# Optimization experiments

Measured on AMD Instinct MI355X. Metric: run time of the kernel, lower is better.

Reference implementation:

```python
import jax, jax.numpy as jnp
import numpy as np

NUM_LAYERS = 2

def setup_inputs() -> dict:
    key = jax.random.key(0)
    ks = jax.random.split(key, 10)
    N, E, V, D, G = 50000, 800000, 100000, 128, 64
    node_ids = jax.random.randint(ks[0], (N,), 0, V)
    edge_index = jax.random.randint(ks[1], (2, E), 0, N)
    batch = jnp.sort(jax.random.randint(ks[2], (N,), 0, G))
    embed = jax.random.normal(ks[3], (V, D), dtype=jnp.float32)
    conv_w = jax.random.normal(ks[4], (NUM_LAYERS, D, D), dtype=jnp.float32) * (1.0 / np.sqrt(D))
    w_ih = jax.random.normal(ks[5], (3 * D, D), dtype=jnp.float32) * (1.0 / np.sqrt(D))
    w_hh = jax.random.normal(ks[6], (3 * D, D), dtype=jnp.float32) * (1.0 / np.sqrt(D))
    b_ih = jax.random.normal(ks[7], (3 * D,), dtype=jnp.float32) * 0.01
    b_hh = jax.random.normal(ks[8], (3 * D,), dtype=jnp.float32) * 0.01
    return {"node_ids": node_ids, "edge_index": edge_index, "batch": batch,
            "num_graphs": 64, "embed": embed, "conv_w": conv_w,
            "w_ih": w_ih, "w_hh": w_hh, "b_ih": b_ih, "b_hh": b_hh}


def _gru_cell(x, h, w_ih, w_hh, b_ih, b_hh):
    # torch.nn.GRUCell math; gate order r, z, n
    gi = x @ w_ih.T + b_ih
    gh = h @ w_hh.T + b_hh
    i_r, i_z, i_n = jnp.split(gi, 3, axis=-1)
    h_r, h_z, h_n = jnp.split(gh, 3, axis=-1)
    r = jax.nn.sigmoid(i_r + h_r)
    z = jax.nn.sigmoid(i_z + h_z)
    n = jnp.tanh(i_n + r * h_n)
    return (1.0 - z) * n + z * h


def reference(node_ids, edge_index, batch, num_graphs, embed, conv_w, w_ih, w_hh, b_ih, b_hh):
    N = node_ids.shape[0]
    src, dst = edge_index[0], edge_index[1]
    h = embed[node_ids]  # [N, D]
    for i in range(NUM_LAYERS):
        m = h @ conv_w[i]                                   # [N, D]
        agg = jax.ops.segment_sum(m[src], dst, num_segments=N)  # scatter-add messages
        h = _gru_cell(agg, h, w_ih, w_hh, b_ih, b_hh)
    # global mean pool per graph
    sums = jax.ops.segment_sum(h, batch, num_segments=num_graphs)       # [G, D]
    counts = jax.ops.segment_sum(jnp.ones((N,), h.dtype), batch, num_segments=num_graphs)
    return sums / jnp.maximum(counts, 1.0)[:, None]
```

## Files before the change

### kernel.cpp

```cpp
#include <hip/hip_runtime.h>
#include <hip/hip_bf16.h>


#define DTHREADS 256
#define BSHIFT 7
#define BNODES 128
#define BCAP 4096

typedef __attribute__((ext_vector_type(8))) short bf16x8;
typedef __attribute__((ext_vector_type(4))) float f32x4;

__device__ __forceinline__ float sigf(float x) { return 1.0f / (1.0f + __expf(-x)); }
__device__ __forceinline__ float tanhfast(float x) { return 1.0f - 2.0f / (1.0f + __expf(2.0f * x)); }

__device__ __forceinline__ unsigned short f2bf_rne(float x) {
  unsigned int u = __float_as_uint(x);
  u += 0x7fff + ((u >> 16) & 1);
  return (unsigned short)(u >> 16);
}
__device__ __forceinline__ float bf2f(unsigned int lo16) {
  return __uint_as_float(lo16 << 16);
}

__global__ __launch_bounds__(DTHREADS) void gather_kernel(
    const float* __restrict__ embed, const int* __restrict__ node_ids,
    unsigned short* __restrict__ hb, int N) {
  int idx = blockIdx.x * DTHREADS + threadIdx.x;
  if (idx >= N * 32) return;
  int n = idx >> 5;
  int c = (idx & 31) * 4;
  int v = node_ids[n];
  float4 val = *(const float4*)&embed[(size_t)v * 128 + c];
  unsigned short b[4] = {f2bf_rne(val.x), f2bf_rne(val.y), f2bf_rne(val.z), f2bf_rne(val.w)};
  *(ushort4*)&hb[(size_t)n * 128 + c] = *(ushort4*)b;
}

__global__ __launch_bounds__(DTHREADS) void pack_all_kernel(
    const float* __restrict__ w_hh, const float* __restrict__ conv_w,
    const float* __restrict__ w_ih, unsigned short* __restrict__ wpk_hh,
    unsigned short* __restrict__ wpk_wc, int nl,
    int* __restrict__ cur, int NB, float* __restrict__ outsum, int osz) {
  int id = blockIdx.x * DTHREADS + threadIdx.x;
  if (id < NB) cur[id] = 0;
  if (id < osz) outsum[id] = 0.f;
  int seg = id / (384 * 128);
  if (seg > nl) return;
  int r = id - seg * (384 * 128);
  int f = r >> 3, i = r & 7;
  int l = f & 63;
  int s = (f >> 6) & 3;
  int t = (f >> 8) & 3;
  int jb = f >> 10;
  int j = jb * 64 + t * 16 + (l & 15);
  int k = s * 32 + (l >> 4) * 8 + i;
  float val;
  unsigned short* dst;
  if (seg == 0) {
    val = w_hh[j * 128 + k];
    dst = wpk_hh;
  } else {
    const float* conv = conv_w + (size_t)(seg - 1) * 128 * 128;
    float acc = 0.f;
    for (int d = 0; d < 128; d += 4) {
      float4 cv = *(const float4*)&conv[k * 128 + d];
      float4 wv = *(const float4*)&w_ih[j * 128 + d];
      acc += cv.x * wv.x + cv.y * wv.y + cv.z * wv.z + cv.w * wv.w;
    }
    val = acc;
    dst = wpk_wc + (size_t)(seg - 1) * 384 * 128;
  }
  dst[(size_t)f * 8 + i] = f2bf_rne(val);
}

__global__ __launch_bounds__(DTHREADS) void bucket_scatter_kernel(
    const int* __restrict__ src, const int* __restrict__ dst,
    int* __restrict__ cur, unsigned int* __restrict__ ebuf, int E, int NB) {
  __shared__ int lc[512];
  __shared__ int lbs[512];
  int tid = threadIdx.x;
  for (int i = tid; i < NB; i += DTHREADS) lc[i] = 0;
  __syncthreads();
  int base = blockIdx.x * 4096;
  int rank[16];
  #pragma unroll
  for (int q = 0; q < 16; ++q) {
    int e = base + q * 256 + tid;
    if (e < E) rank[q] = atomicAdd(&lc[dst[e] >> BSHIFT], 1);
  }
  __syncthreads();
  for (int i = tid; i < NB; i += DTHREADS) {
    int c = lc[i];
    lbs[i] = c ? atomicAdd(&cur[i], c) : 0;
  }
  __syncthreads();
  #pragma unroll
  for (int q = 0; q < 16; ++q) {
    int e = base + q * 256 + tid;
    if (e < E) {
      int d = dst[e];
      int b = d >> BSHIFT;
      int slot = lbs[b] + rank[q];
      if (slot < BCAP)
        ebuf[(size_t)b * BCAP + slot] =
            (unsigned int)src[e] | ((unsigned int)(d & (BNODES - 1)) << 17);
    }
  }
}

__global__ __launch_bounds__(DTHREADS) void bucket_sort_kernel(
    const unsigned int* __restrict__ ebuf, const int* __restrict__ cur,
    int* __restrict__ row_start, int* __restrict__ row_end,
    int* __restrict__ csr_src, int N) {
  __shared__ int cnt[BNODES];
  __shared__ int sc[BNODES];
  const int tid = threadIdx.x;
  const int b = blockIdx.x;
  const int count = min(cur[b], BCAP);
  const unsigned int* eb = ebuf + (size_t)b * BCAP;
  int* cs = csr_src + (size_t)b * BCAP;
  if (tid < BNODES) cnt[tid] = 0;
  __syncthreads();
  for (int i = tid; i < count; i += DTHREADS)
    atomicAdd(&cnt[eb[i] >> 17], 1);
  __syncthreads();
  if (tid < BNODES) sc[tid] = cnt[tid];
  __syncthreads();
  #pragma unroll
  for (int off = 1; off < BNODES; off <<= 1) {
    int t = 0;
    if (tid < BNODES && tid >= off) t = sc[tid - off];
    __syncthreads();
    if (tid < BNODES) sc[tid] += t;
    __syncthreads();
  }
  if (tid < BNODES) {
    int excl = sc[tid] - cnt[tid];
    int n = b * BNODES + tid;
    if (n < N) {
      row_start[n] = b * BCAP + excl;
      row_end[n] = b * BCAP + sc[tid];
    }
    cnt[tid] = excl;
  }
  __syncthreads();
  for (int i = tid; i < count; i += DTHREADS) {
    unsigned int pk = eb[i];
    int slot = atomicAdd(&cnt[pk >> 17], 1);
    cs[slot] = (int)(pk & 0x1FFFFu);
  }
}

__global__ __launch_bounds__(DTHREADS) void aggregate_kernel(
    const unsigned short* __restrict__ hb, const int* __restrict__ row_start,
    const int* __restrict__ row_end, const int* __restrict__ csr_src,
    unsigned short* __restrict__ agg, int N) {
  int node = (blockIdx.x * DTHREADS + threadIdx.x) >> 4;
  if (node >= N) return;
  int c = threadIdx.x & 15;
  int s = row_start[node], e = row_end[node];
  float acc[8] = {0.f, 0.f, 0.f, 0.f, 0.f, 0.f, 0.f, 0.f};
  for (int i = s; i < e; i += 16) {
    int idx[16];
    #pragma unroll
    for (int q = 0; q < 16; ++q) {
      int ii = i + q;
      idx[q] = csr_src[ii < e ? ii : s];
    }
    uint4 d[16];
    #pragma unroll
    for (int q = 0; q < 16; ++q)
      d[q] = *(const uint4*)&hb[(size_t)idx[q] * 128 + c * 8];
    #pragma unroll
    for (int q = 0; q < 16; ++q) {
      if (i + q < e) {
        const unsigned int* dp = (const unsigned int*)&d[q];
        #pragma unroll
        for (int u = 0; u < 4; ++u) {
          acc[2 * u]     += bf2f(dp[u] & 0xffffu);
          acc[2 * u + 1] += bf2f(dp[u] >> 16);
        }
      }
    }
  }
  unsigned int o[4];
  #pragma unroll
  for (int q = 0; q < 4; ++q)
    o[q] = (unsigned int)f2bf_rne(acc[2 * q]) | ((unsigned int)f2bf_rne(acc[2 * q + 1]) << 16);
  *(uint4*)&agg[(size_t)node * 128 + c * 8] = *(uint4*)o;
}

__global__ __launch_bounds__(512, 2) void fused_gru_kernel(
    const unsigned short* __restrict__ aggb, const unsigned short* __restrict__ wpk_wc,
    const unsigned short* __restrict__ wpk_hh, const float* __restrict__ b_ih,
    const float* __restrict__ b_hh, unsigned short* __restrict__ hb,
    int N, int nchunks) {
  __shared__ __align__(16) unsigned short Ag[32 * 128];
  __shared__ __align__(16) unsigned short Hs[32 * 128];
  const int tid = threadIdx.x;
  const int wv = tid >> 6, lane = tid & 63;
  const int lm = lane & 15, quad = lane >> 4;

  bf16x8 BI[3][4], BH[3][4];
  #pragma unroll
  for (int g = 0; g < 3; ++g) {
    int jb = g * 2 + (wv >> 2);
    int t = wv & 3;
    #pragma unroll
    for (int s = 0; s < 4; ++s) {
      size_t f = ((size_t)(jb * 4 + t) * 4 + s) * 64 + lane;
      BI[g][s] = *(const bf16x8*)&wpk_wc[f * 8];
      BH[g][s] = *(const bf16x8*)&wpk_hh[f * 8];
    }
  }

  const int jc = wv * 16 + lm;
  const float bir = b_ih[jc], biz = b_ih[128 + jc], bin_ = b_ih[256 + jc];
  const float bhr = b_hh[jc], bhz = b_hh[128 + jc], bhn = b_hh[256 + jc];
  const int c0 = jc >> 3, ej = jc & 7;

  const int srow = tid >> 4, scol = tid & 15;
  const int sdc = (scol ^ (srow & 15)) * 8;

  int ci = blockIdx.x;
  uint4 va = make_uint4(0, 0, 0, 0), vh = make_uint4(0, 0, 0, 0);
  if (ci < nchunks) {
    int n = ci * 32 + srow;
    if (n < N) {
      va = *(const uint4*)&aggb[(size_t)n * 128 + scol * 8];
      vh = *(const uint4*)&hb[(size_t)n * 128 + scol * 8];
    }
  }

  for (; ci < nchunks; ci += gridDim.x) {
    *(uint4*)&Ag[srow * 128 + sdc] = va;
    *(uint4*)&Hs[srow * 128 + sdc] = vh;
    __syncthreads();

    int cn = ci + gridDim.x;
    va = make_uint4(0, 0, 0, 0); vh = make_uint4(0, 0, 0, 0);
    if (cn < nchunks) {
      int n = cn * 32 + srow;
      if (n < N) {
        va = *(const uint4*)&aggb[(size_t)n * 128 + scol * 8];
        vh = *(const uint4*)&hb[(size_t)n * 128 + scol * 8];
      }
    }

    f32x4 accI[2][3], accH[2][3];
    #pragma unroll
    for (int mi = 0; mi < 2; ++mi)
      #pragma unroll
      for (int g = 0; g < 3; ++g) {
        accI[mi][g] = (f32x4){0.f, 0.f, 0.f, 0.f};
        accH[mi][g] = (f32x4){0.f, 0.f, 0.f, 0.f};
      }

    #pragma unroll
    for (int s = 0; s < 4; ++s) {
      bf16x8 afA[2], afH[2];
      #pragma unroll
      for (int mi = 0; mi < 2; ++mi) {
        int m = mi * 16 + lm;
        int chunk = (s * 4 + quad) ^ (m & 15);
        afA[mi] = *(const bf16x8*)&Ag[m * 128 + chunk * 8];
        afH[mi] = *(const bf16x8*)&Hs[m * 128 + chunk * 8];
      }
      #pragma unroll
      for (int g = 0; g < 3; ++g)
        #pragma unroll
        for (int mi = 0; mi < 2; ++mi) {
          accI[mi][g] = __builtin_amdgcn_mfma_f32_16x16x32_bf16(afA[mi], BI[g][s], accI[mi][g], 0, 0, 0);
          accH[mi][g] = __builtin_amdgcn_mfma_f32_16x16x32_bf16(afH[mi], BH[g][s], accH[mi][g], 0, 0, 0);
        }
    }

    const int n0 = ci * 32;
    #pragma unroll
    for (int mi = 0; mi < 2; ++mi) {
      #pragma unroll
      for (int r = 0; r < 4; ++r) {
        int row = mi * 16 + quad * 4 + r;
        int n = n0 + row;
        if (n >= N) continue;
        float ir = accI[mi][0][r] + bir;
        float iz = accI[mi][1][r] + biz;
        float in_ = accI[mi][2][r] + bin_;
        float hr = accH[mi][0][r] + bhr;
        float hz = accH[mi][1][r] + bhz;
        float hn = accH[mi][2][r] + bhn;
        float rr = sigf(ir + hr);
        float zz = sigf(iz + hz);
        float nn = tanhfast(in_ + rr * hn);
        float hold = bf2f((unsigned int)Hs[row * 128 + ((c0 ^ (row & 15)) * 8) + ej]);
        hb[(size_t)n * 128 + jc] = f2bf_rne((1.f - zz) * nn + zz * hold);
      }
    }
    __syncthreads();
  }
}

__global__ __launch_bounds__(DTHREADS) void pool1_kernel(
    const unsigned short* __restrict__ hb, const int* __restrict__ batch,
    float* __restrict__ outsum, int N) {
  int b = blockIdx.x;
  int c = threadIdx.x & 127;
  int half = threadIdx.x >> 7;
  int nbeg = b * 64;
  int nend = min(nbeg + 64, N);
  float acc = 0.f;
  int cur = -1;
  for (int n = nbeg + half; n < nend; n += 2) {
    int g = batch[n];
    if (g != cur) {
      if (cur >= 0) atomicAdd(&outsum[(size_t)cur * 128 + c], acc);
      acc = 0.f;
      cur = g;
    }
    acc += bf2f((unsigned int)hb[(size_t)n * 128 + c]);
  }
  if (cur >= 0) atomicAdd(&outsum[(size_t)cur * 128 + c], acc);
}

__device__ __forceinline__ int lbound(const int* a, int n, int key) {
  int lo = 0, hi = n;
  while (lo < hi) {
    int mid = (lo + hi) >> 1;
    if (a[mid] < key) lo = mid + 1; else hi = mid;
  }
  return lo;
}

__global__ __launch_bounds__(128) void pool2_kernel(
    const float* __restrict__ outsum, const int* __restrict__ batch,
    float* __restrict__ out, int N) {
  int g = blockIdx.x;
  int c = threadIdx.x;
  int lo = lbound(batch, N, g);
  int hi = lbound(batch, N, g + 1);
  out[(size_t)g * 128 + c] = outsum[(size_t)g * 128 + c] / (float)max(hi - lo, 1);
}

extern "C" void kernel_launch(void* const* d_in, const int* in_sizes, int n_in,
                              void* d_out, int out_size, void* d_ws, size_t ws_size,
                              hipStream_t stream) {
  const int* node_ids = (const int*)d_in[0];
  const int* edge_index = (const int*)d_in[1];
  const int* batch = (const int*)d_in[2];
  const float* embed = (const float*)d_in[4];
  const float* conv_w = (const float*)d_in[5];
  const float* w_ih = (const float*)d_in[6];
  const float* w_hh = (const float*)d_in[7];
  const float* b_ih = (const float*)d_in[8];
  const float* b_hh = (const float*)d_in[9];
  float* out = (float*)d_out;

  const int N = in_sizes[0];
  const int E = in_sizes[1] / 2;
  const int G = out_size / 128;
  const int NUM_LAYERS = in_sizes[5] / (128 * 128);
  const int NB = (N + BNODES - 1) >> BSHIFT;

  const int* e_src = edge_index;
  const int* e_dst = edge_index + E;

  char* p = (char*)d_ws;
  unsigned short* hb = (unsigned short*)p;    p += (size_t)N * 128 * 2;
  unsigned short* aggb = (unsigned short*)p;  p += (size_t)N * 128 * 2;
  float* outsum = (float*)p;                  p += (size_t)G * 128 * 4;
  unsigned short* wpk_hh = (unsigned short*)p; p += (size_t)384 * 128 * 2;
  unsigned short* wpk_wc = (unsigned short*)p; p += (size_t)NUM_LAYERS * 384 * 128 * 2;
  int* cur = (int*)p;        p += 512 * 4;
  int* row_start = (int*)p;  p += (size_t)N * 4;
  int* row_end = (int*)p;    p += (size_t)N * 4;
  unsigned int* ebuf = (unsigned int*)p;  p += (size_t)NB * BCAP * 4;
  int* csr_src = (int*)p;    p += (size_t)NB * BCAP * 4;

  const int nEB = (E + 4095) / 4096;

  {
    int total = (NUM_LAYERS + 1) * 384 * 128;
    pack_all_kernel<<<(total + DTHREADS - 1) / DTHREADS, DTHREADS, 0, stream>>>(
        w_hh, conv_w, w_ih, wpk_hh, wpk_wc, NUM_LAYERS, cur, NB, outsum, G * 128);
  }

  bucket_scatter_kernel<<<nEB, DTHREADS, 0, stream>>>(e_src, e_dst, cur, ebuf, E, NB);
  bucket_sort_kernel<<<NB, DTHREADS, 0, stream>>>(ebuf, cur, row_start, row_end, csr_src, N);

  gather_kernel<<<(N * 32 + DTHREADS - 1) / DTHREADS, DTHREADS, 0, stream>>>(embed, node_ids, hb, N);

  const int nchunks = (N + 31) / 32;
  for (int L = 0; L < NUM_LAYERS; ++L) {
    aggregate_kernel<<<((size_t)N * 16 + DTHREADS - 1) / DTHREADS, DTHREADS, 0, stream>>>(
        hb, row_start, row_end, csr_src, aggb, N);
    fused_gru_kernel<<<512, 512, 0, stream>>>(
        aggb, wpk_wc + (size_t)L * 384 * 128, wpk_hh, b_ih, b_hh, hb, N, nchunks);
  }

  const int pblocks = (N + 63) / 64;
  pool1_kernel<<<pblocks, DTHREADS, 0, stream>>>(hb, batch, outsum, N);
  pool2_kernel<<<G, 128, 0, stream>>>(outsum, batch, out, N);
}
```

Baseline: 286.2 us.

## Store node features in four 32-channel slabs to localize aggregation gathers

```diff
diff --git a/kernel.cpp b/kernel.cpp
--- a/kernel.cpp
+++ b/kernel.cpp
@@ -32,7 +32,7 @@
   int v = node_ids[n];
   float4 val = *(const float4*)&embed[(size_t)v * 128 + c];
   unsigned short b[4] = {f2bf_rne(val.x), f2bf_rne(val.y), f2bf_rne(val.z), f2bf_rne(val.w)};
-  *(ushort4*)&hb[(size_t)n * 128 + c] = *(ushort4*)b;
+  *(ushort4*)&hb[(size_t)(c >> 5) * N * 32 + (size_t)n * 32 + (c & 31)] = *(ushort4*)b;
 }
 
 __global__ __launch_bounds__(DTHREADS) void pack_all_kernel(
@@ -154,9 +154,13 @@
     const unsigned short* __restrict__ hb, const int* __restrict__ row_start,
     const int* __restrict__ row_end, const int* __restrict__ csr_src,
     unsigned short* __restrict__ agg, int N) {
-  int node = (blockIdx.x * DTHREADS + threadIdx.x) >> 4;
+  int x = blockIdx.x & 7;
+  int slab = x >> 1;
+  int unit = (blockIdx.x >> 3) * 2 + (x & 1);
+  int node = unit * 64 + (threadIdx.x >> 2);
   if (node >= N) return;
-  int c = threadIdx.x & 15;
+  int cc = (threadIdx.x & 3) * 8;
+  const unsigned short* hs = hb + (size_t)slab * N * 32;
   int s = row_start[node], e = row_end[node];
   float acc[8] = {0.f, 0.f, 0.f, 0.f, 0.f, 0.f, 0.f, 0.f};
   for (int i = s; i < e; i += 16) {
@@ -169,7 +173,7 @@
     uint4 d[16];
     #pragma unroll
     for (int q = 0; q < 16; ++q)
-      d[q] = *(const uint4*)&hb[(size_t)idx[q] * 128 + c * 8];
+      d[q] = *(const uint4*)&hs[(size_t)idx[q] * 32 + cc];
     #pragma unroll
     for (int q = 0; q < 16; ++q) {
       if (i + q < e) {
@@ -186,7 +190,7 @@
   #pragma unroll
   for (int q = 0; q < 4; ++q)
     o[q] = (unsigned int)f2bf_rne(acc[2 * q]) | ((unsigned int)f2bf_rne(acc[2 * q + 1]) << 16);
-  *(uint4*)&agg[(size_t)node * 128 + c * 8] = *(uint4*)o;
+  *(uint4*)&agg[(size_t)slab * N * 32 + (size_t)node * 32 + cc] = *(uint4*)o;
 }
 
 __global__ __launch_bounds__(512, 2) void fused_gru_kernel(
@@ -217,17 +221,19 @@
   const float bir = b_ih[jc], biz = b_ih[128 + jc], bin_ = b_ih[256 + jc];
   const float bhr = b_hh[jc], bhz = b_hh[128 + jc], bhn = b_hh[256 + jc];
   const int c0 = jc >> 3, ej = jc & 7;
+  const size_t hwoff = (size_t)(jc >> 5) * (size_t)N * 32 + (jc & 31);
 
   const int srow = tid >> 4, scol = tid & 15;
   const int sdc = (scol ^ (srow & 15)) * 8;
+  const size_t sroff = (size_t)(scol >> 2) * (size_t)N * 32 + (scol & 3) * 8;
 
   int ci = blockIdx.x;
   uint4 va = make_uint4(0, 0, 0, 0), vh = make_uint4(0, 0, 0, 0);
   if (ci < nchunks) {
     int n = ci * 32 + srow;
     if (n < N) {
-      va = *(const uint4*)&aggb[(size_t)n * 128 + scol * 8];
-      vh = *(const uint4*)&hb[(size_t)n * 128 + scol * 8];
+      va = *(const uint4*)&aggb[sroff + (size_t)n * 32];
+      vh = *(const uint4*)&hb[sroff + (size_t)n * 32];
     }
   }
 
@@ -241,8 +247,8 @@
     if (cn < nchunks) {
       int n = cn * 32 + srow;
       if (n < N) {
-        va = *(const uint4*)&aggb[(size_t)n * 128 + scol * 8];
-        vh = *(const uint4*)&hb[(size_t)n * 128 + scol * 8];
+        va = *(const uint4*)&aggb[sroff + (size_t)n * 32];
+        vh = *(const uint4*)&hb[sroff + (size_t)n * 32];
       }
     }
 
@@ -292,7 +298,7 @@
         float zz = sigf(iz + hz);
         float nn = tanhfast(in_ + rr * hn);
         float hold = bf2f((unsigned int)Hs[row * 128 + ((c0 ^ (row & 15)) * 8) + ej]);
-        hb[(size_t)n * 128 + jc] = f2bf_rne((1.f - zz) * nn + zz * hold);
+        hb[hwoff + (size_t)n * 32] = f2bf_rne((1.f - zz) * nn + zz * hold);
       }
     }
     __syncthreads();
@@ -305,6 +311,7 @@
   int b = blockIdx.x;
   int c = threadIdx.x & 127;
   int half = threadIdx.x >> 7;
+  const size_t hroff = (size_t)(c >> 5) * (size_t)N * 32 + (c & 31);
   int nbeg = b * 64;
   int nend = min(nbeg + 64, N);
   float acc = 0.f;
@@ -316,7 +323,7 @@
       acc = 0.f;
       cur = g;
     }
-    acc += bf2f((unsigned int)hb[(size_t)n * 128 + c]);
+    acc += bf2f((unsigned int)hb[hroff + (size_t)n * 32]);
   }
   if (cur >= 0) atomicAdd(&outsum[(size_t)cur * 128 + c], acc);
 }
@@ -389,8 +396,10 @@
   gather_kernel<<<(N * 32 + DTHREADS - 1) / DTHREADS, DTHREADS, 0, stream>>>(embed, node_ids, hb, N);
 
   const int nchunks = (N + 31) / 32;
+  const int units = (N + 63) / 64;
+  const int aggblocks = 8 * ((units + 1) / 2);
   for (int L = 0; L < NUM_LAYERS; ++L) {
-    aggregate_kernel<<<((size_t)N * 16 + DTHREADS - 1) / DTHREADS, DTHREADS, 0, stream>>>(
+    aggregate_kernel<<<aggblocks, DTHREADS, 0, stream>>>(
         hb, row_start, row_end, csr_src, aggb, N);
     fused_gru_kernel<<<512, 512, 0, stream>>>(
         aggb, wpk_wc + (size_t)L * 384 * 128, wpk_hh, b_ih, b_hh, hb, N, nchunks);
```

New measurement: 287.5 us. Within noise of the previous version (+0.5%).

## Fuse neighbor aggregation into GRU kernel with ping-pong hidden buffers

Applied to the files above, without the earlier changes.

```diff
diff --git a/kernel.cpp b/kernel.cpp
--- a/kernel.cpp
+++ b/kernel.cpp
@@ -150,50 +150,13 @@
   }
 }
 
-__global__ __launch_bounds__(DTHREADS) void aggregate_kernel(
-    const unsigned short* __restrict__ hb, const int* __restrict__ row_start,
-    const int* __restrict__ row_end, const int* __restrict__ csr_src,
-    unsigned short* __restrict__ agg, int N) {
-  int node = (blockIdx.x * DTHREADS + threadIdx.x) >> 4;
-  if (node >= N) return;
-  int c = threadIdx.x & 15;
-  int s = row_start[node], e = row_end[node];
-  float acc[8] = {0.f, 0.f, 0.f, 0.f, 0.f, 0.f, 0.f, 0.f};
-  for (int i = s; i < e; i += 16) {
-    int idx[16];
-    #pragma unroll
-    for (int q = 0; q < 16; ++q) {
-      int ii = i + q;
-      idx[q] = csr_src[ii < e ? ii : s];
-    }
-    uint4 d[16];
-    #pragma unroll
-    for (int q = 0; q < 16; ++q)
-      d[q] = *(const uint4*)&hb[(size_t)idx[q] * 128 + c * 8];
-    #pragma unroll
-    for (int q = 0; q < 16; ++q) {
-      if (i + q < e) {
-        const unsigned int* dp = (const unsigned int*)&d[q];
-        #pragma unroll
-        for (int u = 0; u < 4; ++u) {
-          acc[2 * u]     += bf2f(dp[u] & 0xffffu);
-          acc[2 * u + 1] += bf2f(dp[u] >> 16);
-        }
-      }
-    }
-  }
-  unsigned int o[4];
-  #pragma unroll
-  for (int q = 0; q < 4; ++q)
-    o[q] = (unsigned int)f2bf_rne(acc[2 * q]) | ((unsigned int)f2bf_rne(acc[2 * q + 1]) << 16);
-  *(uint4*)&agg[(size_t)node * 128 + c * 8] = *(uint4*)o;
-}
-
-__global__ __launch_bounds__(512, 2) void fused_gru_kernel(
-    const unsigned short* __restrict__ aggb, const unsigned short* __restrict__ wpk_wc,
-    const unsigned short* __restrict__ wpk_hh, const float* __restrict__ b_ih,
-    const float* __restrict__ b_hh, unsigned short* __restrict__ hb,
-    int N, int nchunks) {
+__global__ __launch_bounds__(512, 2) void fused_layer_kernel(
+    const unsigned short* __restrict__ hold_buf,
+    const int* __restrict__ row_start, const int* __restrict__ row_end,
+    const int* __restrict__ csr_src,
+    const unsigned short* __restrict__ wpk_wc, const unsigned short* __restrict__ wpk_hh,
+    const float* __restrict__ b_ih, const float* __restrict__ b_hh,
+    unsigned short* __restrict__ hnew_buf, int N, int nchunks) {
   __shared__ __align__(16) unsigned short Ag[32 * 128];
   __shared__ __align__(16) unsigned short Hs[32 * 128];
   const int tid = threadIdx.x;
@@ -221,30 +184,46 @@
   const int srow = tid >> 4, scol = tid & 15;
   const int sdc = (scol ^ (srow & 15)) * 8;
 
-  int ci = blockIdx.x;
-  uint4 va = make_uint4(0, 0, 0, 0), vh = make_uint4(0, 0, 0, 0);
-  if (ci < nchunks) {
+  for (int ci = blockIdx.x; ci < nchunks; ci += gridDim.x) {
     int n = ci * 32 + srow;
+    uint4 va = make_uint4(0, 0, 0, 0), vh = make_uint4(0, 0, 0, 0);
     if (n < N) {
-      va = *(const uint4*)&aggb[(size_t)n * 128 + scol * 8];
-      vh = *(const uint4*)&hb[(size_t)n * 128 + scol * 8];
-    }
-  }
-
-  for (; ci < nchunks; ci += gridDim.x) {
+      int s = row_start[n], e = row_end[n];
+      float acc[8] = {0.f, 0.f, 0.f, 0.f, 0.f, 0.f, 0.f, 0.f};
+      for (int i = s; i < e; i += 8) {
+        int idx[8];
+        #pragma unroll
+        for (int q = 0; q < 8; ++q) {
+          int ii = i + q;
+          idx[q] = csr_src[ii < e ? ii : s];
+        }
+        uint4 d[8];
+        #pragma unroll
+        for (int q = 0; q < 8; ++q)
+          d[q] = *(const uint4*)&hold_buf[(size_t)idx[q] * 128 + scol * 8];
+        #pragma unroll
+        for (int q = 0; q < 8; ++q) {
+          if (i + q < e) {
+            const unsigned int* dp = (const unsigned int*)&d[q];
+            #pragma unroll
+            for (int u = 0; u < 4; ++u) {
+              acc[2 * u]     += bf2f(dp[u] & 0xffffu);
+              acc[2 * u + 1] += bf2f(dp[u] >> 16);
+            }
+          }
+        }
+      }
+      unsigned int o[4];
+      #pragma unroll
+      for (int q = 0; q < 4; ++q)
+        o[q] = (unsigned int)f2bf_rne(acc[2 * q]) | ((unsigned int)f2bf_rne(acc[2 * q + 1]) << 16);
+      va = *(uint4*)o;
+      vh = *(const uint4*)&hold_buf[(size_t)n * 128 + scol * 8];
+    }
+
     *(uint4*)&Ag[srow * 128 + sdc] = va;
     *(uint4*)&Hs[srow * 128 + sdc] = vh;
     __syncthreads();
-
-    int cn = ci + gridDim.x;
-    va = make_uint4(0, 0, 0, 0); vh = make_uint4(0, 0, 0, 0);
-    if (cn < nchunks) {
-      int n = cn * 32 + srow;
-      if (n < N) {
-        va = *(const uint4*)&aggb[(size_t)n * 128 + scol * 8];
-        vh = *(const uint4*)&hb[(size_t)n * 128 + scol * 8];
-      }
-    }
 
     f32x4 accI[2][3], accH[2][3];
     #pragma unroll
@@ -280,8 +259,8 @@
       #pragma unroll
       for (int r = 0; r < 4; ++r) {
         int row = mi * 16 + quad * 4 + r;
-        int n = n0 + row;
-        if (n >= N) continue;
+        int nn = n0 + row;
+        if (nn >= N) continue;
         float ir = accI[mi][0][r] + bir;
         float iz = accI[mi][1][r] + biz;
         float in_ = accI[mi][2][r] + bin_;
@@ -290,9 +269,9 @@
         float hn = accH[mi][2][r] + bhn;
         float rr = sigf(ir + hr);
         float zz = sigf(iz + hz);
-        float nn = tanhfast(in_ + rr * hn);
+        float nn_ = tanhfast(in_ + rr * hn);
         float hold = bf2f((unsigned int)Hs[row * 128 + ((c0 ^ (row & 15)) * 8) + ej]);
-        hb[(size_t)n * 128 + jc] = f2bf_rne((1.f - zz) * nn + zz * hold);
+        hnew_buf[(size_t)nn * 128 + jc] = f2bf_rne((1.f - zz) * nn_ + zz * hold);
       }
     }
     __syncthreads();
@@ -365,7 +344,7 @@
 
   char* p = (char*)d_ws;
   unsigned short* hb = (unsigned short*)p;    p += (size_t)N * 128 * 2;
-  unsigned short* aggb = (unsigned short*)p;  p += (size_t)N * 128 * 2;
+  unsigned short* h2 = (unsigned short*)p;    p += (size_t)N * 128 * 2;
   float* outsum = (float*)p;                  p += (size_t)G * 128 * 4;
   unsigned short* wpk_hh = (unsigned short*)p; p += (size_t)384 * 128 * 2;
   unsigned short* wpk_wc = (unsigned short*)p; p += (size_t)NUM_LAYERS * 384 * 128 * 2;
@@ -390,13 +369,15 @@
 
   const int nchunks = (N + 31) / 32;
   for (int L = 0; L < NUM_LAYERS; ++L) {
-    aggregate_kernel<<<((size_t)N * 16 + DTHREADS - 1) / DTHREADS, DTHREADS, 0, stream>>>(
-        hb, row_start, row_end, csr_src, aggb, N);
-    fused_gru_kernel<<<512, 512, 0, stream>>>(
-        aggb, wpk_wc + (size_t)L * 384 * 128, wpk_hh, b_ih, b_hh, hb, N, nchunks);
-  }
+    const unsigned short* ho = (L & 1) ? h2 : hb;
+    unsigned short* hn = (L & 1) ? hb : h2;
+    fused_layer_kernel<<<512, 512, 0, stream>>>(
+        ho, row_start, row_end, csr_src, wpk_wc + (size_t)L * 384 * 128,
+        wpk_hh, b_ih, b_hh, hn, N, nchunks);
+  }
+  const unsigned short* hfin = (NUM_LAYERS & 1) ? h2 : hb;
 
   const int pblocks = (N + 63) / 64;
-  pool1_kernel<<<pblocks, DTHREADS, 0, stream>>>(hb, batch, outsum, N);
+  pool1_kernel<<<pblocks, DTHREADS, 0, stream>>>(hfin, batch, outsum, N);
   pool2_kernel<<<G, 128, 0, stream>>>(outsum, batch, out, N);
 }
```

Measured after the change: 310.6 us. 8.5% more time.

## Replace bucket-sort CSR build with fixed-capacity per-node adjacency and single-pass pool

Applied to the files above, without the earlier changes.

```diff
diff --git a/kernel.cpp b/kernel.cpp
--- a/kernel.cpp
+++ b/kernel.cpp
@@ -3,9 +3,7 @@
 
 
 #define DTHREADS 256
-#define BSHIFT 7
-#define BNODES 128
-#define BCAP 4096
+#define CAP 64
 
 typedef __attribute__((ext_vector_type(8))) short bf16x8;
 typedef __attribute__((ext_vector_type(4))) float f32x4;
@@ -39,10 +37,9 @@
     const float* __restrict__ w_hh, const float* __restrict__ conv_w,
     const float* __restrict__ w_ih, unsigned short* __restrict__ wpk_hh,
     unsigned short* __restrict__ wpk_wc, int nl,
-    int* __restrict__ cur, int NB, float* __restrict__ outsum, int osz) {
+    int* __restrict__ deg, int N) {
   int id = blockIdx.x * DTHREADS + threadIdx.x;
-  if (id < NB) cur[id] = 0;
-  if (id < osz) outsum[id] = 0.f;
+  if (id < N) deg[id] = 0;
   int seg = id / (384 * 128);
   if (seg > nl) return;
   int r = id - seg * (384 * 128);
@@ -72,99 +69,31 @@
   dst[(size_t)f * 8 + i] = f2bf_rne(val);
 }
 
-__global__ __launch_bounds__(DTHREADS) void bucket_scatter_kernel(
+__global__ __launch_bounds__(DTHREADS) void scatter_direct_kernel(
     const int* __restrict__ src, const int* __restrict__ dst,
-    int* __restrict__ cur, unsigned int* __restrict__ ebuf, int E, int NB) {
-  __shared__ int lc[512];
-  __shared__ int lbs[512];
-  int tid = threadIdx.x;
-  for (int i = tid; i < NB; i += DTHREADS) lc[i] = 0;
-  __syncthreads();
-  int base = blockIdx.x * 4096;
-  int rank[16];
-  #pragma unroll
-  for (int q = 0; q < 16; ++q) {
-    int e = base + q * 256 + tid;
-    if (e < E) rank[q] = atomicAdd(&lc[dst[e] >> BSHIFT], 1);
-  }
-  __syncthreads();
-  for (int i = tid; i < NB; i += DTHREADS) {
-    int c = lc[i];
-    lbs[i] = c ? atomicAdd(&cur[i], c) : 0;
-  }
-  __syncthreads();
-  #pragma unroll
-  for (int q = 0; q < 16; ++q) {
-    int e = base + q * 256 + tid;
-    if (e < E) {
-      int d = dst[e];
-      int b = d >> BSHIFT;
-      int slot = lbs[b] + rank[q];
-      if (slot < BCAP)
-        ebuf[(size_t)b * BCAP + slot] =
-            (unsigned int)src[e] | ((unsigned int)(d & (BNODES - 1)) << 17);
-    }
-  }
-}
-
-__global__ __launch_bounds__(DTHREADS) void bucket_sort_kernel(
-    const unsigned int* __restrict__ ebuf, const int* __restrict__ cur,
-    int* __restrict__ row_start, int* __restrict__ row_end,
-    int* __restrict__ csr_src, int N) {
-  __shared__ int cnt[BNODES];
-  __shared__ int sc[BNODES];
-  const int tid = threadIdx.x;
-  const int b = blockIdx.x;
-  const int count = min(cur[b], BCAP);
-  const unsigned int* eb = ebuf + (size_t)b * BCAP;
-  int* cs = csr_src + (size_t)b * BCAP;
-  if (tid < BNODES) cnt[tid] = 0;
-  __syncthreads();
-  for (int i = tid; i < count; i += DTHREADS)
-    atomicAdd(&cnt[eb[i] >> 17], 1);
-  __syncthreads();
-  if (tid < BNODES) sc[tid] = cnt[tid];
-  __syncthreads();
-  #pragma unroll
-  for (int off = 1; off < BNODES; off <<= 1) {
-    int t = 0;
-    if (tid < BNODES && tid >= off) t = sc[tid - off];
-    __syncthreads();
-    if (tid < BNODES) sc[tid] += t;
-    __syncthreads();
-  }
-  if (tid < BNODES) {
-    int excl = sc[tid] - cnt[tid];
-    int n = b * BNODES + tid;
-    if (n < N) {
-      row_start[n] = b * BCAP + excl;
-      row_end[n] = b * BCAP + sc[tid];
-    }
-    cnt[tid] = excl;
-  }
-  __syncthreads();
-  for (int i = tid; i < count; i += DTHREADS) {
-    unsigned int pk = eb[i];
-    int slot = atomicAdd(&cnt[pk >> 17], 1);
-    cs[slot] = (int)(pk & 0x1FFFFu);
-  }
+    int* __restrict__ deg, int* __restrict__ csr, int E) {
+  int e = blockIdx.x * DTHREADS + threadIdx.x;
+  if (e >= E) return;
+  int d = dst[e];
+  int slot = atomicAdd(&deg[d], 1);
+  if (slot < CAP) csr[(size_t)d * CAP + slot] = src[e];
 }
 
 __global__ __launch_bounds__(DTHREADS) void aggregate_kernel(
-    const unsigned short* __restrict__ hb, const int* __restrict__ row_start,
-    const int* __restrict__ row_end, const int* __restrict__ csr_src,
-    unsigned short* __restrict__ agg, int N) {
+    const unsigned short* __restrict__ hb, const int* __restrict__ deg,
+    const int* __restrict__ csr, unsigned short* __restrict__ agg, int N) {
   int node = (blockIdx.x * DTHREADS + threadIdx.x) >> 4;
   if (node >= N) return;
   int c = threadIdx.x & 15;
-  int s = row_start[node], e = row_end[node];
+  int e = min(deg[node], CAP);
+  const int* cs = csr + (size_t)node * CAP;
   float acc[8] = {0.f, 0.f, 0.f, 0.f, 0.f, 0.f, 0.f, 0.f};
-  for (int i = s; i < e; i += 16) {
+  for (int i = 0; i < e; i += 16) {
     int idx[16];
     #pragma unroll
     for (int q = 0; q < 16; ++q) {
       int ii = i + q;
-      idx[q] = csr_src[ii < e ? ii : s];
+      idx[q] = cs[ii < e ? ii : 0];
     }
     uint4 d[16];
     #pragma unroll
@@ -299,28 +228,6 @@
   }
 }
 
-__global__ __launch_bounds__(DTHREADS) void pool1_kernel(
-    const unsigned short* __restrict__ hb, const int* __restrict__ batch,
-    float* __restrict__ outsum, int N) {
-  int b = blockIdx.x;
-  int c = threadIdx.x & 127;
-  int half = threadIdx.x >> 7;
-  int nbeg = b * 64;
-  int nend = min(nbeg + 64, N);
-  float acc = 0.f;
-  int cur = -1;
-  for (int n = nbeg + half; n < nend; n += 2) {
-    int g = batch[n];
-    if (g != cur) {
-      if (cur >= 0) atomicAdd(&outsum[(size_t)cur * 128 + c], acc);
-      acc = 0.f;
-      cur = g;
-    }
-    acc += bf2f((unsigned int)hb[(size_t)n * 128 + c]);
-  }
-  if (cur >= 0) atomicAdd(&outsum[(size_t)cur * 128 + c], acc);
-}
-
 __device__ __forceinline__ int lbound(const int* a, int n, int key) {
   int lo = 0, hi = n;
   while (lo < hi) {
@@ -330,14 +237,34 @@
   return lo;
 }
 
-__global__ __launch_bounds__(128) void pool2_kernel(
-    const float* __restrict__ outsum, const int* __restrict__ batch,
+__global__ __launch_bounds__(512) void pool_kernel(
+    const unsigned short* __restrict__ hb, const int* __restrict__ batch,
     float* __restrict__ out, int N) {
+  __shared__ float red[32 * 128];
   int g = blockIdx.x;
-  int c = threadIdx.x;
   int lo = lbound(batch, N, g);
   int hi = lbound(batch, N, g + 1);
-  out[(size_t)g * 128 + c] = outsum[(size_t)g * 128 + c] / (float)max(hi - lo, 1);
+  int t = threadIdx.x;
+  int grp = t >> 4, lane = t & 15;
+  float a[8] = {0.f, 0.f, 0.f, 0.f, 0.f, 0.f, 0.f, 0.f};
+  for (int n = lo + grp; n < hi; n += 32) {
+    uint4 v = *(const uint4*)&hb[(size_t)n * 128 + lane * 8];
+    const unsigned int* dp = (const unsigned int*)&v;
+    #pragma unroll
+    for (int u = 0; u < 4; ++u) {
+      a[2 * u]     += bf2f(dp[u] & 0xffffu);
+      a[2 * u + 1] += bf2f(dp[u] >> 16);
+    }
+  }
+  #pragma unroll
+  for (int u = 0; u < 8; ++u) red[grp * 128 + lane * 8 + u] = a[u];
+  __syncthreads();
+  if (t < 128) {
+    float s = 0.f;
+    #pragma unroll
+    for (int q = 0; q < 32; ++q) s += red[q * 128 + t];
+    out[(size_t)g * 128 + t] = s / (float)max(hi - lo, 1);
+  }
 }
 
 extern "C" void kernel_launch(void* const* d_in, const int* in_sizes, int n_in,
@@ -358,7 +285,6 @@
   const int E = in_sizes[1] / 2;
   const int G = out_size / 128;
   const int NUM_LAYERS = in_sizes[5] / (128 * 128);
-  const int NB = (N + BNODES - 1) >> BSHIFT;
 
   const int* e_src = edge_index;
   const int* e_dst = edge_index + E;
@@ -366,37 +292,29 @@
   char* p = (char*)d_ws;
   unsigned short* hb = (unsigned short*)p;    p += (size_t)N * 128 * 2;
   unsigned short* aggb = (unsigned short*)p;  p += (size_t)N * 128 * 2;
-  float* outsum = (float*)p;                  p += (size_t)G * 128 * 4;
   unsigned short* wpk_hh = (unsigned short*)p; p += (size_t)384 * 128 * 2;
   unsigned short* wpk_wc = (unsigned short*)p; p += (size_t)NUM_LAYERS * 384 * 128 * 2;
-  int* cur = (int*)p;        p += 512 * 4;
-  int* row_start = (int*)p;  p += (size_t)N * 4;
-  int* row_end = (int*)p;    p += (size_t)N * 4;
-  unsigned int* ebuf = (unsigned int*)p;  p += (size_t)NB * BCAP * 4;
-  int* csr_src = (int*)p;    p += (size_t)NB * BCAP * 4;
-
-  const int nEB = (E + 4095) / 4096;
+  int* deg = (int*)p;        p += (size_t)N * 4;
+  int* csr = (int*)p;        p += (size_t)N * CAP * 4;
 
   {
     int total = (NUM_LAYERS + 1) * 384 * 128;
     pack_all_kernel<<<(total + DTHREADS - 1) / DTHREADS, DTHREADS, 0, stream>>>(
-        w_hh, conv_w, w_ih, wpk_hh, wpk_wc, NUM_LAYERS, cur, NB, outsum, G * 128);
-  }
-
-  bucket_scatter_kernel<<<nEB, DTHREADS, 0, stream>>>(e_src, e_dst, cur, ebuf, E, NB);
-  bucket_sort_kernel<<<NB, DTHREADS, 0, stream>>>(ebuf, cur, row_start, row_end, csr_src, N);
+        w_hh, conv_w, w_ih, wpk_hh, wpk_wc, NUM_LAYERS, deg, N);
+  }
+
+  scatter_direct_kernel<<<(E + DTHREADS - 1) / DTHREADS, DTHREADS, 0, stream>>>(
+      e_src, e_dst, deg, csr, E);
 
   gather_kernel<<<(N * 32 + DTHREADS - 1) / DTHREADS, DTHREADS, 0, stream>>>(embed, node_ids, hb, N);
 
   const int nchunks = (N + 31) / 32;
   for (int L = 0; L < NUM_LAYERS; ++L) {
     aggregate_kernel<<<((size_t)N * 16 + DTHREADS - 1) / DTHREADS, DTHREADS, 0, stream>>>(
-        hb, row_start, row_end, csr_src, aggb, N);
+        hb, deg, csr, aggb, N);
     fused_gru_kernel<<<512, 512, 0, stream>>>(
         aggb, wpk_wc + (size_t)L * 384 * 128, wpk_hh, b_ih, b_hh, hb, N, nchunks);
   }
 
-  const int pblocks = (N + 63) / 64;
-  pool1_kernel<<<pblocks, DTHREADS, 0, stream>>>(hb, batch, outsum, N);
-  pool2_kernel<<<G, 128, 0, stream>>>(outsum, batch, out, N);
-}
+  pool_kernel<<<G, 512, 0, stream>>>(hb, batch, out, N);
+}
```

Measured after the change: 291.9 us. No clear change (+2.0%).
